# Kernel optimization log

Hardware: AMD Instinct MI355X
Metric: run time of the kernel (lower is better)

The kernel has to match this reference:

```python
import jax, jax.numpy as jnp
import numpy as np

N_NODES = 32767   # complete binary tree, depth 15
EMB_DIM = 256
HIDDEN = 256      # 'hidden_size' -> LSTM state is 2*HIDDEN
VOCAB = 32        # len(ExprNode.TYPE_LIST)


def setup_inputs() -> dict:
    key = jax.random.key(0)
    k1, k2, k3, k4, k5, k6 = jax.random.split(key, 6)
    H2 = 2 * HIDDEN
    types = jax.random.randint(k1, (N_NODES,), 0, VOCAB, dtype=jnp.int32)
    # complete binary tree: children of node i are 2i+1 / 2i+2; sentinel slot N = zero state
    idx = np.arange(N_NODES)
    a = 2 * idx + 1
    b = 2 * idx + 2
    a = np.where(a < N_NODES, a, N_NODES).astype(np.int32)
    b = np.where(b < N_NODES, b, N_NODES).astype(np.int32)
    scale = 1.0 / np.sqrt(H2)
    return {
        "types": types,
        "a_idx": jnp.asarray(a),
        "b_idx": jnp.asarray(b),
        "emb": jax.random.normal(k2, (VOCAB, EMB_DIM), jnp.float32) * 0.02,
        "W_ih": jax.random.normal(k3, (4 * H2, EMB_DIM), jnp.float32) * scale,
        "W_hh": jax.random.normal(k4, (4 * H2, H2), jnp.float32) * scale,
        "b_ih": jax.random.normal(k5, (4 * H2,), jnp.float32) * scale,
        "b_hh": jax.random.normal(k6, (4 * H2,), jnp.float32) * scale,
    }


def reference(types, a_idx, b_idx, emb, W_ih, W_hh, b_ih, b_hh):
    """Recursive binary tree-LSTM over topological (leaves-first) order.
    Each node's LSTM state has size 2H; a parent's incoming (h, c) is the concat
    of the first H entries of each child's state (zeros for missing children).
    Returns per-node hidden outputs [N, 2H] (the out_map, indexed by node id)."""
    N = types.shape[0]
    H2 = W_hh.shape[1]
    H = H2 // 2
    # batched input projection for all nodes at once: [N, 4*H2]
    x_proj = emb[types] @ W_ih.T + (b_ih + b_hh)
    Hs0 = jnp.zeros((N + 1, H2), x_proj.dtype)  # slot N = h0 (zeros)
    Cs0 = jnp.zeros((N + 1, H2), x_proj.dtype)
    order = jnp.arange(N - 1, -1, -1)  # children (higher index) before parents

    def step(carry, i):
        Hs, Cs = carry
        h = jnp.concatenate([Hs[a_idx[i], :H], Hs[b_idx[i], :H]])  # [2H]
        c = jnp.concatenate([Cs[a_idx[i], :H], Cs[b_idx[i], :H]])
        gates = x_proj[i] + W_hh @ h                 # [4*H2], torch gate order i,f,g,o
        ig, fg, gg, og = jnp.split(gates, 4)
        c_new = jax.nn.sigmoid(fg) * c + jax.nn.sigmoid(ig) * jnp.tanh(gg)
        h_new = jax.nn.sigmoid(og) * jnp.tanh(c_new)
        return (Hs.at[i].set(h_new), Cs.at[i].set(c_new)), h_new

    _, outs = jax.lax.scan(step, (Hs0, Cs0), order)
    return outs[::-1]  # reorder so row i is node i's output
```

## Files before the change

### kernel.cpp

```cpp
#include <hip/hip_runtime.h>
#include <hip/hip_bf16.h>


#define NNODES 32767

typedef __attribute__((ext_vector_type(8))) short bf16x8;
typedef __attribute__((ext_vector_type(4))) float f32x4;

typedef const __attribute__((address_space(1))) void* gptr_t;
typedef __attribute__((address_space(3))) void* lptr_t;

__device__ __forceinline__ float sigf(float x) { return 1.0f / (1.0f + __expf(-x)); }
__device__ __forceinline__ float tanhfast(float x) { return 2.0f / (1.0f + __expf(-2.0f * x)) - 1.0f; }

__device__ __forceinline__ short bf_hi(float x) {
    __hip_bfloat16 h = __float2bfloat16(x);
    return __builtin_bit_cast(short, h);
}
__device__ __forceinline__ float bf_f(short s) {
    __hip_bfloat16 h = __builtin_bit_cast(__hip_bfloat16, s);
    return __bfloat162float(h);
}
__device__ __forceinline__ void split8(const float* src, short* hi, short* lo) {
#pragma unroll
    for (int j = 0; j < 8; ++j) {
        float x = src[j];
        short h = bf_hi(x);
        hi[j] = h;
        lo[j] = bf_hi(x - bf_f(h));
    }
}

__global__ void proj_kernel(const float* __restrict__ emb, const float* __restrict__ W_ih,
                            const float* __restrict__ b_ih, const float* __restrict__ b_hh,
                            float* __restrict__ proj) {
    __shared__ float e[256];
    int v = blockIdx.x >> 3;
    int rc = blockIdx.x & 7;
    int t = threadIdx.x;
    e[t] = emb[v * 256 + t];
    __syncthreads();
    int r = rc * 256 + t;
    const float4* w4 = (const float4*)(W_ih + (size_t)r * 256);
    const float4* e4 = (const float4*)e;
    float acc = 0.f;
#pragma unroll 8
    for (int k = 0; k < 64; ++k) {
        float4 w = w4[k];
        float4 h = e4[k];
        acc += w.x * h.x + w.y * h.y + w.z * h.z + w.w * h.w;
    }
    proj[v * 2048 + r] = acc + b_ih[r] + b_hh[r];
}

__global__ void wpack_kernel(const float* __restrict__ W_hh,
                             short* __restrict__ Whi, short* __restrict__ Wlo) {
    int t = blockIdx.x * 256 + threadIdx.x;
    int lane = t & 63;
    int kt = (t >> 6) & 15;
    int ntile = t >> 10;
    int n = ntile * 16 + (lane & 15);
    int k0 = kt * 32 + (lane >> 4) * 8;
    const float* src = W_hh + (size_t)n * 512 + k0;
    short hi[8], lo[8];
    split8(src, hi, lo);
    *(bf16x8*)(Whi + (size_t)t * 8) = *(bf16x8*)hi;
    *(bf16x8*)(Wlo + (size_t)t * 8) = *(bf16x8*)lo;
}

__global__ void leaf_kernel(const int* __restrict__ types, const float* __restrict__ proj,
                            float* __restrict__ out, float* __restrict__ C256,
                            short* __restrict__ Hsplit) {
    int bi = blockIdx.x;
    int node = 16383 + (bi >> 1);
    int j = ((bi & 1) << 8) + threadIdx.x;
    int tt = types[node];
    const float* p = proj + (size_t)tt * 2048;
    float gi = p[j];
    float gg = p[1024 + j];
    float go = p[1536 + j];
    float cn = sigf(gi) * tanhfast(gg);
    float hn = sigf(go) * tanhfast(cn);
    out[(size_t)node * 512 + j] = hn;
    if ((bi & 1) == 0) {
        C256[(size_t)node * 256 + j] = cn;
        short hi = bf_hi(hn);
        Hsplit[(size_t)node * 512 + j] = hi;
        Hsplit[(size_t)node * 512 + 256 + j] = bf_hi(hn - bf_f(hi));
    }
}

__global__ __launch_bounds__(256) void big_gemm_lstm_kernel(
    const int* __restrict__ a_idx, const int* __restrict__ b_idx,
    const int* __restrict__ types, float* __restrict__ out,
    const float* __restrict__ proj, float* __restrict__ C256,
    short* __restrict__ Hsplit, int node_base) {
    __shared__ __align__(16) short lds[2][16384];
    __shared__ int sA[128], sB[128], sT[128];

    const unsigned WOFF = 16777216u;

    int t = threadIdx.x;
    int lin = blockIdx.x;
    int x = lin >> 4;
    int y = (lin & 7) * 2 + ((lin >> 3) & 1);
    int node0 = node_base + x * 128;
    int j0 = y * 32;

    if (t < 128) {
        sA[t] = a_idx[node0 + t];
        sB[t] = b_idx[node0 + t];
        sT[t] = types[node0 + t];
    }
    __syncthreads();

    int w = t >> 6, lane = t & 63;
    int wm = w >> 1, wn = w & 1;

    unsigned b0[8], b1[8], sk;
    if (w < 2) {
        sk = 32u;
#pragma unroll
        for (int i = 0; i < 8; ++i) {
            int ca = w * 8 + i;
            int rl = lane >> 3;
            int r_loc = ca * 8 + rl;
            int j = (lane & 7) ^ rl;
            unsigned ks = (unsigned)(j >> 2) * 256u + (unsigned)(j & 3) * 8u;
            b0[i] = (unsigned)sA[r_loc] * 512u + ks;
            b1[i] = (unsigned)sB[r_loc] * 512u + ks;
        }
    } else {
        sk = 512u;
#pragma unroll
        for (int i = 0; i < 8; ++i) {
            int cc = (w - 2) * 8 + i;
            int nt = cc >> 1, part = cc & 1;
            int q = nt >> 1, sub = nt & 1;
            unsigned ntg = (unsigned)(q * 32 + y * 2 + sub);
            b0[i] = WOFF + ntg * 8192u + (unsigned)part * 1048576u + (unsigned)lane * 8u;
            b1[i] = b0[i] + 4096u;
        }
    }

    f32x4 acc[4][4];
#pragma unroll
    for (int i = 0; i < 4; ++i)
#pragma unroll
        for (int q = 0; q < 4; ++q) acc[i][q] = (f32x4){0.f, 0.f, 0.f, 0.f};

    auto stage = [&](int kt, int buf) {
#pragma unroll
        for (int i = 0; i < 8; ++i) {
            unsigned off = ((kt < 8) ? b0[i] : b1[i]) + (unsigned)(kt & 7) * sk;
            const short* gsrc = Hsplit + off;
            short* ldst = &lds[buf][(w * 8 + i) * 512];
            __builtin_amdgcn_global_load_lds((gptr_t)gsrc, (lptr_t)ldst, 16, 0, 0);
        }
    };

    auto compute = [&](int buf) {
        const short* L = lds[buf];
        int s = lane >> 4;
        bf16x8 ah[4], al[4];
#pragma unroll
        for (int i = 0; i < 4; ++i) {
            int m_loc = (wm * 4 + i) * 16 + (lane & 15);
            int ch = m_loc >> 3;
            int r = m_loc & 7;
            const short* base = L + ch * 512 + r * 64;
            ah[i] = *(const bf16x8*)&base[(s ^ r) * 8];
            al[i] = *(const bf16x8*)&base[((4 + s) ^ r) * 8];
        }
        __builtin_amdgcn_s_setprio(1);
#pragma unroll
        for (int q = 0; q < 4; ++q) {
            int nt = q * 2 + wn;
            bf16x8 bh = *(const bf16x8*)&L[(16 + nt * 2) * 512 + lane * 8];
            bf16x8 bl = *(const bf16x8*)&L[(17 + nt * 2) * 512 + lane * 8];
#pragma unroll
            for (int i = 0; i < 4; ++i) {
                acc[i][q] = __builtin_amdgcn_mfma_f32_16x16x32_bf16(ah[i], bh, acc[i][q], 0, 0, 0);
                acc[i][q] = __builtin_amdgcn_mfma_f32_16x16x32_bf16(ah[i], bl, acc[i][q], 0, 0, 0);
                acc[i][q] = __builtin_amdgcn_mfma_f32_16x16x32_bf16(al[i], bh, acc[i][q], 0, 0, 0);
            }
        }
        __builtin_amdgcn_s_setprio(0);
    };

    stage(0, 0);
    int cur = 0;
#pragma unroll 1
    for (int kt = 0; kt < 16; ++kt) {
        __builtin_amdgcn_s_barrier();
        if (kt < 15) stage(kt + 1, cur ^ 1);
        if (kt < 15) {
            asm volatile("s_waitcnt vmcnt(8)" ::: "memory");
        } else {
            asm volatile("s_waitcnt vmcnt(0)" ::: "memory");
        }
        __builtin_amdgcn_s_barrier();
        compute(cur);
        cur ^= 1;
    }

    int j = j0 + wn * 16 + (lane & 15);
    bool fh = (j < 256);
    int jc = j & 255;
#pragma unroll
    for (int i = 0; i < 4; ++i) {
        int mrow = wm * 64 + i * 16 + (lane >> 4) * 4;
#pragma unroll
        for (int r = 0; r < 4; ++r) {
            int m_loc = mrow + r;
            int node = node0 + m_loc;
            const float* p = proj + (size_t)sT[m_loc] * 2048 + j;
            float gi = acc[i][0][r] + p[0];
            float gf = acc[i][1][r] + p[512];
            float gg = acc[i][2][r] + p[1024];
            float go = acc[i][3][r] + p[1536];
            int child = fh ? sA[m_loc] : sB[m_loc];
            float c = C256[(size_t)child * 256 + jc];
            float cn = sigf(gf) * c + sigf(gi) * tanhfast(gg);
            float hn = sigf(go) * tanhfast(cn);
            out[(size_t)node * 512 + j] = hn;
            if (fh) {
                C256[(size_t)node * 256 + j] = cn;
                short hi = bf_hi(hn);
                Hsplit[(size_t)node * 512 + j] = hi;
                Hsplit[(size_t)node * 512 + 256 + j] = bf_hi(hn - bf_f(hi));
            }
        }
    }
}

__global__ __launch_bounds__(256) void gemm_lstm_kernel(
    const int* __restrict__ a_idx, const int* __restrict__ b_idx,
    const int* __restrict__ types, float* __restrict__ out,
    const short* __restrict__ Whi, const short* __restrict__ Wlo,
    const float* __restrict__ proj, float* __restrict__ C256,
    short* __restrict__ Hsplit, int node_base, int Jc) {
    __shared__ short Ahi[2][16][64][8];
    __shared__ short Alo[2][16][64][8];
    __shared__ int sA[32], sB[32], sT[32];
    int t = threadIdx.x;
    int node0 = node_base + blockIdx.x * 32;
    if (t < 32) {
        sA[t] = a_idx[node0 + t];
        sB[t] = b_idx[node0 + t];
        sT[t] = types[node0 + t];
    }
    __syncthreads();

#pragma unroll
    for (int it = 0; it < 8; ++it) {
        int c = it * 256 + t;
        int mt = c >> 10;
        int kt = (c >> 6) & 15;
        int lane = c & 63;
        int m_loc = mt * 16 + (lane & 15);
        int k0 = kt * 32 + (lane >> 4) * 8;
        int child = (k0 < 256) ? sA[m_loc] : sB[m_loc];
        const short* src = Hsplit + (size_t)child * 512 + (k0 & 255);
        *(bf16x8*)&Ahi[mt][kt][lane][0] = *(const bf16x8*)src;
        *(bf16x8*)&Alo[mt][kt][lane][0] = *(const bf16x8*)(src + 256);
    }
    __syncthreads();

    int w = t >> 6;
    int lane = t & 63;
    int jsteps = Jc >> 4;
    int jbase = blockIdx.y * Jc;

    auto epilogue = [&](int j0, f32x4 (&acc)[4][2]) {
        int j = j0 + (lane & 15);
        int jc = j & 255;
        bool fh = (j < 256);
#pragma unroll
        for (int mt = 0; mt < 2; ++mt) {
            int mrow = mt * 16 + (lane >> 4) * 4;
#pragma unroll
            for (int r = 0; r < 4; ++r) {
                int m_loc = mrow + r;
                int node = node0 + m_loc;
                const float* p = proj + (size_t)sT[m_loc] * 2048 + j;
                float gi = acc[0][mt][r] + p[0];
                float gf = acc[1][mt][r] + p[512];
                float gg = acc[2][mt][r] + p[1024];
                float go = acc[3][mt][r] + p[1536];
                int child = fh ? sA[m_loc] : sB[m_loc];
                float c = C256[(size_t)child * 256 + jc];
                float cn = sigf(gf) * c + sigf(gi) * tanhfast(gg);
                float hn = sigf(go) * tanhfast(cn);
                out[(size_t)node * 512 + j] = hn;
                if (fh) {
                    C256[(size_t)node * 256 + j] = cn;
                    short hi = bf_hi(hn);
                    Hsplit[(size_t)node * 512 + j] = hi;
                    Hsplit[(size_t)node * 512 + 256 + j] = bf_hi(hn - bf_f(hi));
                }
            }
        }
    };

    if (jsteps >= 4) {
        for (int js = w; js < jsteps; js += 4) {
            int j0 = jbase + js * 16;
            f32x4 acc[4][2];
#pragma unroll
            for (int q = 0; q < 4; ++q)
#pragma unroll
                for (int mt = 0; mt < 2; ++mt) acc[q][mt] = (f32x4){0.f, 0.f, 0.f, 0.f};
            int nt0 = j0 >> 4;
#pragma unroll 4
            for (int kt = 0; kt < 16; ++kt) {
                bf16x8 ah0 = *(const bf16x8*)&Ahi[0][kt][lane][0];
                bf16x8 al0 = *(const bf16x8*)&Alo[0][kt][lane][0];
                bf16x8 ah1 = *(const bf16x8*)&Ahi[1][kt][lane][0];
                bf16x8 al1 = *(const bf16x8*)&Alo[1][kt][lane][0];
#pragma unroll
                for (int q = 0; q < 4; ++q) {
                    int ntile = q * 32 + nt0;
                    size_t off = ((size_t)(ntile * 16 + kt) * 64 + lane) * 8;
                    bf16x8 bh = *(const bf16x8*)(Whi + off);
                    bf16x8 bl = *(const bf16x8*)(Wlo + off);
                    acc[q][0] = __builtin_amdgcn_mfma_f32_16x16x32_bf16(ah0, bh, acc[q][0], 0, 0, 0);
                    acc[q][0] = __builtin_amdgcn_mfma_f32_16x16x32_bf16(ah0, bl, acc[q][0], 0, 0, 0);
                    acc[q][0] = __builtin_amdgcn_mfma_f32_16x16x32_bf16(al0, bh, acc[q][0], 0, 0, 0);
                    acc[q][1] = __builtin_amdgcn_mfma_f32_16x16x32_bf16(ah1, bh, acc[q][1], 0, 0, 0);
                    acc[q][1] = __builtin_amdgcn_mfma_f32_16x16x32_bf16(ah1, bl, acc[q][1], 0, 0, 0);
                    acc[q][1] = __builtin_amdgcn_mfma_f32_16x16x32_bf16(al1, bh, acc[q][1], 0, 0, 0);
                }
            }
            epilogue(j0, acc);
        }
    } else {
        int js = w & 1;
        int khalf = w >> 1;
        int j0 = jbase + js * 16;
        f32x4 acc[4][2];
#pragma unroll
        for (int q = 0; q < 4; ++q)
#pragma unroll
            for (int mt = 0; mt < 2; ++mt) acc[q][mt] = (f32x4){0.f, 0.f, 0.f, 0.f};
        int nt0 = j0 >> 4;
        int kt0 = khalf * 8;
#pragma unroll 4
        for (int kt = kt0; kt < kt0 + 8; ++kt) {
            bf16x8 ah0 = *(const bf16x8*)&Ahi[0][kt][lane][0];
            bf16x8 al0 = *(const bf16x8*)&Alo[0][kt][lane][0];
            bf16x8 ah1 = *(const bf16x8*)&Ahi[1][kt][lane][0];
            bf16x8 al1 = *(const bf16x8*)&Alo[1][kt][lane][0];
#pragma unroll
            for (int q = 0; q < 4; ++q) {
                int ntile = q * 32 + nt0;
                size_t off = ((size_t)(ntile * 16 + kt) * 64 + lane) * 8;
                bf16x8 bh = *(const bf16x8*)(Whi + off);
                bf16x8 bl = *(const bf16x8*)(Wlo + off);
                acc[q][0] = __builtin_amdgcn_mfma_f32_16x16x32_bf16(ah0, bh, acc[q][0], 0, 0, 0);
                acc[q][0] = __builtin_amdgcn_mfma_f32_16x16x32_bf16(ah0, bl, acc[q][0], 0, 0, 0);
                acc[q][0] = __builtin_amdgcn_mfma_f32_16x16x32_bf16(al0, bh, acc[q][0], 0, 0, 0);
                acc[q][1] = __builtin_amdgcn_mfma_f32_16x16x32_bf16(ah1, bh, acc[q][1], 0, 0, 0);
                acc[q][1] = __builtin_amdgcn_mfma_f32_16x16x32_bf16(ah1, bl, acc[q][1], 0, 0, 0);
                acc[q][1] = __builtin_amdgcn_mfma_f32_16x16x32_bf16(al1, bh, acc[q][1], 0, 0, 0);
            }
        }
        __syncthreads();
        float* xch = (float*)&Ahi[0][0][0][0];
        if (khalf == 1) {
#pragma unroll
            for (int q = 0; q < 4; ++q)
#pragma unroll
                for (int mt = 0; mt < 2; ++mt)
                    *(f32x4*)&xch[(((q * 2 + mt) * 128) + js * 64 + lane) * 4] = acc[q][mt];
        }
        __syncthreads();
        if (khalf == 0) {
#pragma unroll
            for (int q = 0; q < 4; ++q)
#pragma unroll
                for (int mt = 0; mt < 2; ++mt) {
                    f32x4 o = *(const f32x4*)&xch[(((q * 2 + mt) * 128) + js * 64 + lane) * 4];
                    acc[q][mt] += o;
                }
            epilogue(j0, acc);
        }
    }
}

__global__ __launch_bounds__(256) void smallv2_gemm_kernel(
    const int* __restrict__ a_idx, const int* __restrict__ b_idx,
    const float* __restrict__ out, const short* __restrict__ Whi,
    float* __restrict__ part, int node_base, int B) {
    __shared__ float hs[16][64];
    const short* Wlo = Whi + 1048576;

    int t = threadIdx.x;
    int y = blockIdx.x, z = blockIdx.y;
    int r = y * 256 + t;
    int kbase = z * 64;

    if (t < B * 16) {
        int n = t >> 4;
        int f4 = t & 15;
        int node = node_base + n;
        int child = (kbase < 256) ? a_idx[node] : b_idx[node];
        float4 v = ((const float4*)(out + (size_t)child * 512 + (kbase & 255)))[f4];
        *(float4*)&hs[n][f4 * 4] = v;
    }
    __syncthreads();

    float wv[64];
#pragma unroll
    for (int u = 0; u < 8; ++u) {
        int k = kbase + u * 8;
        int kt = k >> 5;
        int sub = (k >> 3) & 3;
        size_t off = ((size_t)((r >> 4) * 16 + kt) * 64 + (sub << 4) + (r & 15)) * 8;
        bf16x8 hi = *(const bf16x8*)(Whi + off);
        bf16x8 lo = *(const bf16x8*)(Wlo + off);
#pragma unroll
        for (int e = 0; e < 8; ++e)
            wv[u * 8 + e] = bf_f(hi[e]) + bf_f(lo[e]);
    }

    for (int n = 0; n < B; ++n) {
        float acc = 0.f;
#pragma unroll
        for (int k = 0; k < 64; ++k) acc += wv[k] * hs[n][k];
        part[((size_t)z * B + n) * 2048 + r] = acc;
    }
}

__global__ void small_combine_kernel(
    const int* __restrict__ a_idx, const int* __restrict__ b_idx,
    const int* __restrict__ types, const float* __restrict__ part,
    const float* __restrict__ proj, float* __restrict__ C256,
    short* __restrict__ Hsplit, float* __restrict__ out, int node_base, int B) {
    int bi = blockIdx.x;
    int n = bi >> 1;
    int j = ((bi & 1) << 8) + threadIdx.x;
    int node = node_base + n;
    float g[4] = {0.f, 0.f, 0.f, 0.f};
    for (int z = 0; z < 8; ++z) {
        const float* p = part + ((size_t)z * B + n) * 2048;
#pragma unroll
        for (int q = 0; q < 4; ++q) g[q] += p[q * 512 + j];
    }
    const float* p = proj + (size_t)types[node] * 2048 + j;
    float gi = g[0] + p[0];
    float gf = g[1] + p[512];
    float gg = g[2] + p[1024];
    float go = g[3] + p[1536];
    int child = (j < 256) ? a_idx[node] : b_idx[node];
    float c = C256[(size_t)child * 256 + (j & 255)];
    float cn = sigf(gf) * c + sigf(gi) * tanhfast(gg);
    float hn = sigf(go) * tanhfast(cn);
    out[(size_t)node * 512 + j] = hn;
    if (j < 256) {
        C256[(size_t)node * 256 + j] = cn;
        short hi = bf_hi(hn);
        Hsplit[(size_t)node * 512 + j] = hi;
        Hsplit[(size_t)node * 512 + 256 + j] = bf_hi(hn - bf_f(hi));
    }
}

extern "C" void kernel_launch(void* const* d_in, const int* in_sizes, int n_in,
                              void* d_out, int out_size, void* d_ws, size_t ws_size,
                              hipStream_t stream) {
    const int* types = (const int*)d_in[0];
    const int* a_idx = (const int*)d_in[1];
    const int* b_idx = (const int*)d_in[2];
    const float* emb = (const float*)d_in[3];
    const float* W_ih = (const float*)d_in[4];
    const float* W_hh = (const float*)d_in[5];
    const float* b_ih = (const float*)d_in[6];
    const float* b_hh = (const float*)d_in[7];
    float* out = (float*)d_out;

    float* ws = (float*)d_ws;
    float* proj = ws;
    float* C256 = ws + 65536;
    short* Hsplit = (short*)(C256 + 8388352);
    short* Whi = Hsplit + 16777216;
    short* Wlo = Whi + 1048576;
    float* part = (float*)(Wlo + 1048576);

    proj_kernel<<<256, 256, 0, stream>>>(emb, W_ih, b_ih, b_hh, proj);
    wpack_kernel<<<512, 256, 0, stream>>>(W_hh, Whi, Wlo);
    leaf_kernel<<<32768, 256, 0, stream>>>(types, proj, out, C256, Hsplit);

    for (int d = 13; d >= 0; --d) {
        int base = (1 << d) - 1;
        int B = 1 << d;
        if (B >= 1024) {
            int X = B / 128;
            big_gemm_lstm_kernel<<<X * 16, 256, 0, stream>>>(
                a_idx, b_idx, types, out, proj, C256, Hsplit, base);
        } else if (B >= 32) {
            int bx = B / 32;
            int J = 2;
            while (bx * J < 512 && J < 16) J <<= 1;
            gemm_lstm_kernel<<<dim3(bx, J), 256, 0, stream>>>(
                a_idx, b_idx, types, out, Whi, Wlo, proj, C256, Hsplit, base, 512 / J);
        } else {
            smallv2_gemm_kernel<<<dim3(8, 8), 256, 0, stream>>>(
                a_idx, b_idx, out, Whi, part, base, B);
            small_combine_kernel<<<B * 2, 256, 0, stream>>>(
                a_idx, b_idx, types, part, proj, C256, Hsplit, out, base, B);
        }
    }
}
```

Before: 402.0 us.

## Halve leaf grid, remap big GEMM blocks per XCD, raise big-kernel threshold

The leaf kernel now handles both halves of a node's 512-wide state in one block, halving the block count and removing the branch on block parity. The big GEMM-LSTM kernel's block-to-tile mapping now keeps all 16 column tiles of a node group on the same XCD (lin&7), so those blocks share L2 for the gathered child states. The depth with 1024 nodes now goes to the mid-size gemm_lstm_kernel instead of the big one. These are three independent scheduling tweaks whose benefits depend on L2 locality and per-level occupancy.

```diff
diff --git a/kernel.cpp b/kernel.cpp
--- a/kernel.cpp
+++ b/kernel.cpp
@@ -71,23 +71,26 @@
 __global__ void leaf_kernel(const int* __restrict__ types, const float* __restrict__ proj,
                             float* __restrict__ out, float* __restrict__ C256,
                             short* __restrict__ Hsplit) {
-    int bi = blockIdx.x;
-    int node = 16383 + (bi >> 1);
-    int j = ((bi & 1) << 8) + threadIdx.x;
+    int node = 16383 + blockIdx.x;
+    int t = threadIdx.x;
     int tt = types[node];
     const float* p = proj + (size_t)tt * 2048;
-    float gi = p[j];
-    float gg = p[1024 + j];
-    float go = p[1536 + j];
+    float gi = p[t];
+    float gg = p[1024 + t];
+    float go = p[1536 + t];
     float cn = sigf(gi) * tanhfast(gg);
     float hn = sigf(go) * tanhfast(cn);
-    out[(size_t)node * 512 + j] = hn;
-    if ((bi & 1) == 0) {
-        C256[(size_t)node * 256 + j] = cn;
-        short hi = bf_hi(hn);
-        Hsplit[(size_t)node * 512 + j] = hi;
-        Hsplit[(size_t)node * 512 + 256 + j] = bf_hi(hn - bf_f(hi));
-    }
+    out[(size_t)node * 512 + t] = hn;
+    C256[(size_t)node * 256 + t] = cn;
+    short hi = bf_hi(hn);
+    Hsplit[(size_t)node * 512 + t] = hi;
+    Hsplit[(size_t)node * 512 + 256 + t] = bf_hi(hn - bf_f(hi));
+    float gi2 = p[256 + t];
+    float gg2 = p[1280 + t];
+    float go2 = p[1792 + t];
+    float cn2 = sigf(gi2) * tanhfast(gg2);
+    float hn2 = sigf(go2) * tanhfast(cn2);
+    out[(size_t)node * 512 + 256 + t] = hn2;
 }
 
 __global__ __launch_bounds__(256) void big_gemm_lstm_kernel(
@@ -102,8 +105,10 @@
 
     int t = threadIdx.x;
     int lin = blockIdx.x;
-    int x = lin >> 4;
-    int y = (lin & 7) * 2 + ((lin >> 3) & 1);
+    int xcd = lin & 7;
+    int g = lin >> 3;
+    int y = g & 15;
+    int x = (g >> 4) * 8 + xcd;
     int node0 = node_base + x * 128;
     int j0 = y * 32;
 
@@ -488,12 +493,12 @@
 
     proj_kernel<<<256, 256, 0, stream>>>(emb, W_ih, b_ih, b_hh, proj);
     wpack_kernel<<<512, 256, 0, stream>>>(W_hh, Whi, Wlo);
-    leaf_kernel<<<32768, 256, 0, stream>>>(types, proj, out, C256, Hsplit);
+    leaf_kernel<<<16384, 256, 0, stream>>>(types, proj, out, C256, Hsplit);
 
     for (int d = 13; d >= 0; --d) {
         int base = (1 << d) - 1;
         int B = 1 << d;
-        if (B >= 1024) {
+        if (B >= 2048) {
             int X = B / 128;
             big_gemm_lstm_kernel<<<X * 16, 256, 0, stream>>>(
                 a_idx, b_idx, types, out, proj, C256, Hsplit, base);
```

New measurement: 385.1 us. 1.04x faster.
